# Kernel optimization log

Hardware: AMD Instinct MI355X
Metric: run time of the kernel (lower is better)

## Reference

```python
import math
import jax, jax.numpy as jnp
import numpy as np

D = 1024
NH = 16
DH = D // NH


def setup_inputs() -> dict:
    key = jax.random.key(0)
    k1, k2, k3 = jax.random.split(key, 3)
    x = jax.random.normal(k1, (2, 2048, D), dtype=jnp.float32)
    s = 1.0 / math.sqrt(D)
    W_qkv = jax.random.normal(k2, (D, 3 * D), dtype=jnp.float32) * s
    W_o = jax.random.normal(k3, (D, D), dtype=jnp.float32) * s
    return {"x": x, "W_qkv": W_qkv, "W_o": W_o}


def _rope(q, k, base=10000.0):
    # q, k: [B, H, T, dh]
    half = q.shape[-1] // 2
    freqs = jnp.arange(half, dtype=q.dtype) / half
    theta = 1.0 / base ** freqs                      # [half]
    t = jnp.arange(q.shape[-2], dtype=q.dtype)       # [T]
    ang = t[:, None] * theta[None, :]                # [T, half]
    cos = jnp.cos(ang)[None, None, :, :]
    sin = jnp.sin(ang)[None, None, :, :]

    def rot(x):
        x1, x2 = x[..., :half], x[..., half:]
        return jnp.concatenate([x1 * cos - x2 * sin, x1 * sin + x2 * cos], axis=-1)

    return rot(q), rot(k)


def reference(x, W_qkv, W_o):
    B, T, d = x.shape
    qkv = x @ W_qkv                                   # [B, T, 3D]
    q, k, v = jnp.split(qkv, 3, axis=-1)
    q = q.reshape(B, T, NH, DH).transpose(0, 2, 1, 3)  # [B, H, T, dh]
    k = k.reshape(B, T, NH, DH).transpose(0, 2, 1, 3)
    v = v.reshape(B, T, NH, DH).transpose(0, 2, 1, 3)
    q, k = _rope(q, k)
    att = jnp.einsum('bhtd,bhsd->bhts', q, k) / math.sqrt(DH)  # [B, H, T, T]
    mask = jnp.triu(jnp.full((T, T), -jnp.inf, dtype=att.dtype), 1)
    att = att + mask
    w = jax.nn.softmax(att, axis=-1)
    y = jnp.einsum('bhts,bhsd->bhtd', w, v)           # [B, H, T, dh]
    y = y.transpose(0, 2, 1, 3).reshape(B, T, d)
    return y @ W_o
```

## Files before the change

### kernel.cpp

```cpp
#include <hip/hip_runtime.h>

typedef __bf16 bf16x8 __attribute__((ext_vector_type(8)));
typedef float f32x4 __attribute__((ext_vector_type(4)));
typedef float f32x16 __attribute__((ext_vector_type(16)));

constexpr int SEQ = 2048;
constexpr int DMODEL = 1024;

#define GLL(gp, lp)                                                              \
  __builtin_amdgcn_global_load_lds((const __attribute__((address_space(1))) void*)(gp), \
                                   (__attribute__((address_space(3))) void*)(lp), 16, 0, 0)

__global__ __launch_bounds__(256) void prep_kernel(const float* __restrict__ x,
                                                   const float* __restrict__ Wqkv,
                                                   const float* __restrict__ Wo,
                                                   __bf16* __restrict__ xbf,
                                                   __bf16* __restrict__ WqkvT,
                                                   __bf16* __restrict__ WoT,
                                                   float2* __restrict__ sct) {
  __shared__ __bf16 tile[64][72];
  int blk = blockIdx.x, t = threadIdx.x;

  if (blk < 256) {
    int i = blk * 256 + t;
    int tt = i >> 5, j = i & 31;
    float theta = exp2f(-(float)j * 0.41524101186092953f);
    float s, c;
    __sincosf((float)tt * theta, &s, &c);
    sct[i] = make_float2(c, s);
    return;
  }
  if (blk >= 1280) {
    size_t i = (size_t)(blk - 1280) * 256 + t;
    const float* sp = x + i * 8;
    float4 f0 = *reinterpret_cast<const float4*>(sp);
    float4 f1 = *reinterpret_cast<const float4*>(sp + 4);
    alignas(16) __bf16 tmp[8];
    tmp[0] = (__bf16)f0.x; tmp[1] = (__bf16)f0.y; tmp[2] = (__bf16)f0.z; tmp[3] = (__bf16)f0.w;
    tmp[4] = (__bf16)f1.x; tmp[5] = (__bf16)f1.y; tmp[6] = (__bf16)f1.z; tmp[7] = (__bf16)f1.w;
    *reinterpret_cast<uint4*>(xbf + i * 8) = *reinterpret_cast<const uint4*>(tmp);
    return;
  }
  const float* src;
  __bf16* dst;
  int C, R, c0, r0;
  if (blk < 512) {
    int idx = blk - 256;
    src = Wo; dst = WoT; R = 1024; C = 1024;
    c0 = (idx & 15) * 64; r0 = (idx >> 4) * 64;
  } else {
    int idx = blk - 512;
    src = Wqkv; dst = WqkvT; R = 1024; C = 3072;
    c0 = (idx % 48) * 64; r0 = (idx / 48) * 64;
  }
#pragma unroll
  for (int p = 0; p < 2; ++p) {
    int flat = p * 256 + t;
    int i = flat >> 3;
    int j8 = (flat & 7) * 8;
    const float* sp = &src[(size_t)(r0 + i) * C + c0 + j8];
    float4 f0 = *reinterpret_cast<const float4*>(sp);
    float4 f1 = *reinterpret_cast<const float4*>(sp + 4);
    tile[i][j8 + 0] = (__bf16)f0.x; tile[i][j8 + 1] = (__bf16)f0.y;
    tile[i][j8 + 2] = (__bf16)f0.z; tile[i][j8 + 3] = (__bf16)f0.w;
    tile[i][j8 + 4] = (__bf16)f1.x; tile[i][j8 + 5] = (__bf16)f1.y;
    tile[i][j8 + 6] = (__bf16)f1.z; tile[i][j8 + 7] = (__bf16)f1.w;
  }
  __syncthreads();
#pragma unroll
  for (int p = 0; p < 2; ++p) {
    int flat = p * 256 + t;
    int i = flat >> 3;
    int j8 = (flat & 7) * 8;
    alignas(16) __bf16 tmp[8];
#pragma unroll
    for (int jj = 0; jj < 8; ++jj) tmp[jj] = tile[j8 + jj][i];
    *reinterpret_cast<uint4*>(&dst[(size_t)(c0 + i) * R + r0 + j8]) =
        *reinterpret_cast<const uint4*>(tmp);
  }
}

template <typename CT, int BN, int MODE>
__global__ __launch_bounds__(512, 6) void gemm_bt_lds(const __bf16* __restrict__ A,
                                                      const __bf16* __restrict__ BT,
                                                      CT* __restrict__ C,
                                                      int M, int N, int K, int lda, int ldc,
                                                      const float2* __restrict__ sct,
                                                      __bf16* __restrict__ vt) {
  constexpr int NF = BN / 32;
  __shared__ __align__(16) __bf16 AB_lds[128 + BN][64];
  __bf16 (*A_lds)[64] = &AB_lds[0];
  __bf16 (*B_lds)[64] = &AB_lds[128];

  int tid = threadIdx.x;
  int lane = tid & 63, w = tid >> 6;
  int g = lane >> 4, l15 = lane & 15;
  int wr = w & 3;
  int wc = w >> 2;
  int m0 = blockIdx.x * 128;
  int n0 = blockIdx.y * BN;
  int r8 = lane >> 3;
  int cxe = 8 * ((lane & 7) ^ r8);

  const __bf16* ag = A + (size_t)(m0 + w * 16 + r8) * lda + cxe;
  const __bf16* bg = BT + (size_t)(n0 + w * (BN / 8) + r8) * K + cxe;

  int sxa = 8 * (l15 & 7);

  f32x4 acc[2][NF] = {};

  for (int k0 = 0; k0 < K; k0 += 64) {
    __syncthreads();
    GLL(ag + k0, &A_lds[w * 16][0]);
    GLL(ag + (size_t)8 * lda + k0, &A_lds[w * 16 + 8][0]);
    if constexpr (BN == 128) {
      GLL(bg + k0, &B_lds[w * 16][0]);
      GLL(bg + (size_t)8 * K + k0, &B_lds[w * 16 + 8][0]);
    } else {
      GLL(bg + k0, &B_lds[w * 8][0]);
    }
    __syncthreads();
#pragma unroll
    for (int kk = 0; kk < 2; ++kk) {
      int col = (kk * 32 + g * 8) ^ sxa;
      bf16x8 a[2], bb[NF];
#pragma unroll
      for (int m = 0; m < 2; ++m)
        a[m] = *reinterpret_cast<const bf16x8*>(&A_lds[wr * 32 + m * 16 + l15][col]);
#pragma unroll
      for (int n = 0; n < NF; ++n)
        bb[n] = *reinterpret_cast<const bf16x8*>(&B_lds[wc * (BN / 2) + n * 16 + l15][col]);
#pragma unroll
      for (int m = 0; m < 2; ++m)
#pragma unroll
        for (int n = 0; n < NF; ++n)
          acc[m][n] = __builtin_amdgcn_mfma_f32_16x16x32_bf16(a[m], bb[n], acc[m][n], 0, 0, 0);
    }
  }

  if constexpr (MODE == 3) {
    if (n0 >= 2048) {
      __bf16 (*T_lds)[72] = reinterpret_cast<__bf16(*)[72]>(&AB_lds[0][0]);
      int b = m0 >> 11;
      int s_base = m0 & (SEQ - 1);
#pragma unroll
      for (int half = 0; half < 2; ++half) {
        __syncthreads();
        if (wc == half) {
#pragma unroll
          for (int m = 0; m < 2; ++m)
#pragma unroll
            for (int n = 0; n < NF; ++n)
#pragma unroll
              for (int r = 0; r < 4; ++r)
                T_lds[wr * 32 + m * 16 + 4 * g + r][n * 16 + l15] = (__bf16)acc[m][n][r];
        }
        __syncthreads();
        int head = ((n0 - 2048) >> 6) + half;
        int bh = b * 16 + head;
        int d = tid >> 3;
        int s8 = (tid & 7) * 16;
        __bf16* dst = vt + (size_t)bh * 64 * SEQ + (size_t)d * SEQ + s_base + s8;
#pragma unroll
        for (int j = 0; j < 2; ++j) {
          alignas(16) __bf16 tmp[8];
#pragma unroll
          for (int e = 0; e < 8; ++e) tmp[e] = T_lds[s8 + j * 8 + e][d];
          *reinterpret_cast<uint4*>(dst + j * 8) = *reinterpret_cast<const uint4*>(tmp);
        }
      }
      return;
    }
    bool isq = (n0 < 1024);
    float sc = isq ? 0.18033688011112042f : 1.0f;
#pragma unroll
    for (int m = 0; m < 2; ++m)
#pragma unroll
      for (int r = 0; r < 4; ++r) {
        int row = m0 + wr * 32 + m * 16 + 4 * g + r;
        int t = row & (SEQ - 1);
#pragma unroll
        for (int n = 0; n < 2; ++n) {
          int j = n * 16 + l15;
          float2 cs = sct[(t << 5) + j];
          float x1 = acc[m][n][r], x2 = acc[m][n + 2][r];
          acc[m][n][r]     = (x1 * cs.x - x2 * cs.y) * sc;
          acc[m][n + 2][r] = (x1 * cs.y + x2 * cs.x) * sc;
        }
      }
  }

#pragma unroll
  for (int m = 0; m < 2; ++m)
#pragma unroll
    for (int n = 0; n < NF; ++n)
#pragma unroll
      for (int r = 0; r < 4; ++r) {
        int row = m0 + wr * 32 + m * 16 + 4 * g + r;
        int col = n0 + wc * (BN / 2) + n * 16 + l15;
        C[(size_t)row * ldc + col] = (CT)acc[m][n][r];
      }
}

__device__ inline uint32_t pkbf(float a, float b) {
  union { __bf16 h[2]; uint32_t u; } z;
  z.h[0] = (__bf16)a; z.h[1] = (__bf16)b;
  return z.u;
}

__device__ inline __bf16* slot_base(int gi, __bf16* qkv, __bf16* xbf, int q_local) {
  if (gi < 1024)
    return qkv + (size_t)(gi * 4 + (q_local >> 4)) * 3072 + 2048 + (q_local & 15) * 64;
  return xbf + (size_t)(gi - 1024) * 4096 + (size_t)q_local * 64;
}

__global__ __launch_bounds__(128, 3) void attn_kernel(__bf16* __restrict__ qkv,
                                                      const __bf16* __restrict__ vt,
                                                      __bf16* __restrict__ xbf,
                                                      float* __restrict__ pml) {
  __shared__ __align__(16) __bf16 K_lds[2][64][64];

  int tid = threadIdx.x;
  int w = tid >> 6, lane = tid & 63;
  int l31 = lane & 31, hi = lane >> 5;
  int bid = blockIdx.x;
  int it = bid >> 5, bh = bid & 31;
  int b = bh >> 4, h = bh & 15;

  int qc = 31 - (it >> 1);
  int half = it & 1;
  int NTf = qc + 1;
  int hs = (NTf + 1) >> 1;
  int kv0 = half ? hs : 0;
  int kv1 = half ? NTf : hs;
  int NT = kv1 - kv0;

  __bf16* qbase = qkv + (size_t)b * SEQ * 3072 + h * 64;
  const __bf16* kbase = qbase + 1024;
  const __bf16* vtb = vt + (size_t)bh * 64 * SEQ;

  int q_g = qc * 64 + w * 32 + l31;

  int r8 = lane >> 3;
  int cxe = 8 * ((lane & 7) ^ r8);

  auto STAGE = [&](int bufv, int t) {
#pragma unroll
    for (int i = 0; i < 4; ++i) {
      int R = w * 32 + i * 8;
      GLL(kbase + (size_t)(t * 64 + R + r8) * 3072 + cxe, &K_lds[bufv][R][0]);
    }
  };

  bf16x8 qf[4];
#pragma unroll
  for (int ds = 0; ds < 4; ++ds)
    qf[ds] = *reinterpret_cast<const bf16x8*>(qbase + (size_t)q_g * 3072 + ds * 16 + 8 * hi);

  f32x16 oacc[2] = {};
  float l_run = 0.f;
  const float MFIX = 8.0f;

  if (NT > 0) STAGE(0, kv0);
  __syncthreads();

  int buf = 0;
  for (int jb = 0; jb < NT; ++jb) {
    int kt_g = kv0 + jb;
    bool pre = (jb + 1 < NT);
    if (pre) STAGE(buf ^ 1, kt_g + 1);

    uint4 vr[8];
#pragma unroll
    for (int dt = 0; dt < 2; ++dt)
#pragma unroll
      for (int ks = 0; ks < 4; ++ks)
        vr[dt * 4 + ks] = *reinterpret_cast<const uint4*>(
            vtb + (size_t)(dt * 32 + l31) * SEQ + kt_g * 64 + ks * 16 + 8 * hi);

    f32x16 sacc[2] = {};
    __builtin_amdgcn_s_setprio(1);
#pragma unroll
    for (int kt = 0; kt < 2; ++kt) {
#pragma unroll
      for (int ds = 0; ds < 4; ++ds) {
        bf16x8 kf = *reinterpret_cast<const bf16x8*>(
            &K_lds[buf][kt * 32 + l31][(ds * 16 + 8 * hi) ^ ((l31 & 7) * 8)]);
        sacc[kt] = __builtin_amdgcn_mfma_f32_32x32x16_bf16(kf, qf[ds], sacc[kt], 0, 0, 0);
      }
    }
    __builtin_amdgcn_s_setprio(0);

    if (kt_g == qc) {
#pragma unroll
      for (int kt = 0; kt < 2; ++kt)
#pragma unroll
        for (int r = 0; r < 16; ++r) {
          int k_g = kt_g * 64 + kt * 32 + (r & 3) + 8 * (r >> 2) + 4 * hi;
          if (k_g > q_g) sacc[kt][r] = -1e30f;
        }
    }

    float s0 = 0.f, s1 = 0.f, s2 = 0.f, s3 = 0.f;
#pragma unroll
    for (int kt = 0; kt < 2; ++kt) {
#pragma unroll
      for (int r = 0; r < 16; r += 4) {
        float p0 = exp2f(sacc[kt][r + 0] - MFIX);
        float p1 = exp2f(sacc[kt][r + 1] - MFIX);
        float p2 = exp2f(sacc[kt][r + 2] - MFIX);
        float p3 = exp2f(sacc[kt][r + 3] - MFIX);
        sacc[kt][r + 0] = p0; sacc[kt][r + 1] = p1;
        sacc[kt][r + 2] = p2; sacc[kt][r + 3] = p3;
        s0 += p0; s1 += p1; s2 += p2; s3 += p3;
      }
    }
    float sum = (s0 + s1) + (s2 + s3);
    sum += __shfl_xor(sum, 32);
    l_run += sum;

    uint4 pa[4];
#pragma unroll
    for (int ks = 0; ks < 4; ++ks) {
      int v0 = 2 * ks, v1 = v0 + 1;
      int t0 = v0 >> 2, rb0 = 4 * (v0 & 3);
      int t1 = v1 >> 2, rb1 = 4 * (v1 & 3);
      uint32_t a01, a23, b01, b23;
      if (t0 == 0) { a01 = pkbf(sacc[0][rb0 + 0], sacc[0][rb0 + 1]);
                     a23 = pkbf(sacc[0][rb0 + 2], sacc[0][rb0 + 3]); }
      else         { a01 = pkbf(sacc[1][rb0 + 0], sacc[1][rb0 + 1]);
                     a23 = pkbf(sacc[1][rb0 + 2], sacc[1][rb0 + 3]); }
      if (t1 == 0) { b01 = pkbf(sacc[0][rb1 + 0], sacc[0][rb1 + 1]);
                     b23 = pkbf(sacc[0][rb1 + 2], sacc[0][rb1 + 3]); }
      else         { b01 = pkbf(sacc[1][rb1 + 0], sacc[1][rb1 + 1]);
                     b23 = pkbf(sacc[1][rb1 + 2], sacc[1][rb1 + 3]); }
      uint32_t t01 = hi ? a01 : b01;
      uint32_t t23 = hi ? a23 : b23;
      uint32_t r01 = __shfl_xor(t01, 32);
      uint32_t r23 = __shfl_xor(t23, 32);
      uint32_t k01 = hi ? b01 : a01;
      uint32_t k23 = hi ? b23 : a23;
      pa[ks].x = hi ? r01 : k01;
      pa[ks].y = hi ? r23 : k23;
      pa[ks].z = hi ? k01 : r01;
      pa[ks].w = hi ? k23 : r23;
    }

    __builtin_amdgcn_s_setprio(1);
#pragma unroll
    for (int dt = 0; dt < 2; ++dt) {
#pragma unroll
      for (int ks = 0; ks < 4; ++ks) {
        oacc[dt] = __builtin_amdgcn_mfma_f32_32x32x16_bf16(
            *reinterpret_cast<const bf16x8*>(&vr[dt * 4 + ks]),
            *reinterpret_cast<const bf16x8*>(&pa[ks]), oacc[dt], 0, 0, 0);
      }
    }
    __builtin_amdgcn_s_setprio(0);

    if (pre) {
      asm volatile("s_waitcnt vmcnt(0)" ::: "memory");
      __syncthreads();
    }
    buf ^= 1;
  }

  int gi = ((31 - qc) * 2 + half) * 32 + bh;
  int q_local = w * 32 + l31;
  __bf16* pobase = slot_base(gi, qkv, xbf, q_local);
#pragma unroll
  for (int dt = 0; dt < 2; ++dt)
#pragma unroll
    for (int u = 0; u < 4; ++u) {
      int d0 = dt * 32 + 8 * u + 4 * hi;
      alignas(8) __bf16 tmp[4];
#pragma unroll
      for (int m = 0; m < 4; ++m) tmp[m] = (__bf16)oacc[dt][4 * u + m];
      *reinterpret_cast<uint2*>(pobase + d0) = *reinterpret_cast<const uint2*>(tmp);
    }
  if (hi == 0) pml[gi * 128 + q_local] = l_run;
}

__global__ __launch_bounds__(128) void combine_kernel(__bf16* __restrict__ qkv,
                                                      __bf16* __restrict__ xbf,
                                                      const float* __restrict__ pml) {
  int bid = blockIdx.x;
  int qc = 31 - (bid >> 5), bh = bid & 31;
  int b = bh >> 4, h = bh & 15;
  int t = threadIdx.x;
  int q = t >> 1, dh = (t & 1) * 32;

  int g0 = ((31 - qc) * 2 + 0) * 32 + bh;
  int g1 = g0 + 32;
  float l0 = pml[g0 * 128 + q];
  float l1 = pml[g1 * 128 + q];
  float inv = 1.0f / (l0 + l1);

  const __bf16* p0 = slot_base(g0, qkv, xbf, q) + dh;
  const __bf16* p1 = slot_base(g1, qkv, xbf, q) + dh;
  __bf16* yq = qkv + (size_t)(b * SEQ + qc * 64 + q) * 3072 + h * 64 + dh;

#pragma unroll
  for (int c = 0; c < 4; ++c) {
    uint4 ua = *reinterpret_cast<const uint4*>(p0 + c * 8);
    uint4 ub = *reinterpret_cast<const uint4*>(p1 + c * 8);
    const __bf16* va = reinterpret_cast<const __bf16*>(&ua);
    const __bf16* vb = reinterpret_cast<const __bf16*>(&ub);
    alignas(16) __bf16 outv[8];
#pragma unroll
    for (int j = 0; j < 8; ++j)
      outv[j] = (__bf16)((((float)va[j]) + ((float)vb[j])) * inv);
    *reinterpret_cast<uint4*>(yq + c * 8) = *reinterpret_cast<const uint4*>(outv);
  }
}

extern "C" void kernel_launch(void* const* d_in, const int* in_sizes, int n_in,
                              void* d_out, int out_size, void* d_ws, size_t ws_size,
                              hipStream_t stream) {
  const float* x = (const float*)d_in[0];
  const float* Wqkv = (const float*)d_in[1];
  const float* Wo = (const float*)d_in[2];
  float* out = (float*)d_out;

  __bf16* ws = (__bf16*)d_ws;
  __bf16* WqkvT = ws;
  __bf16* WoT = WqkvT + (size_t)3072 * 1024;
  __bf16* qkv = WoT + (size_t)1024 * 1024;
  __bf16* xbf = qkv + (size_t)4096 * 3072;
  __bf16* vtb = xbf + (size_t)4096 * 1024;
  float* pml = (float*)(vtb + (size_t)32 * 64 * SEQ);
  float2* sct = (float2*)(pml + 2048 * 128);

  prep_kernel<<<3328, 256, 0, stream>>>(x, Wqkv, Wo, xbf, WqkvT, WoT, sct);

  gemm_bt_lds<__bf16, 128, 3><<<dim3(32, 24), 512, 0, stream>>>(
      xbf, WqkvT, qkv, 4096, 3072, 1024, 1024, 3072, sct, vtb);

  attn_kernel<<<2048, 128, 0, stream>>>(qkv, vtb, xbf, pml);

  combine_kernel<<<1024, 128, 0, stream>>>(qkv, xbf, pml);

  gemm_bt_lds<float, 64, 0><<<dim3(32, 16), 512, 0, stream>>>(
      qkv, WoT, out, 4096, 1024, 1024, 3072, 1024, sct, nullptr);
}
```

Before: 118.8 us.

## Load K tiles directly from global into registers, drop LDS double buffer

```diff
diff --git a/kernel.cpp b/kernel.cpp
--- a/kernel.cpp
+++ b/kernel.cpp
@@ -214,12 +214,10 @@
   return xbf + (size_t)(gi - 1024) * 4096 + (size_t)q_local * 64;
 }
 
-__global__ __launch_bounds__(128, 3) void attn_kernel(__bf16* __restrict__ qkv,
+__global__ __launch_bounds__(128, 4) void attn_kernel(__bf16* __restrict__ qkv,
                                                       const __bf16* __restrict__ vt,
                                                       __bf16* __restrict__ xbf,
                                                       float* __restrict__ pml) {
-  __shared__ __align__(16) __bf16 K_lds[2][64][64];
-
   int tid = threadIdx.x;
   int w = tid >> 6, lane = tid & 63;
   int l31 = lane & 31, hi = lane >> 5;
@@ -241,17 +239,6 @@
 
   int q_g = qc * 64 + w * 32 + l31;
 
-  int r8 = lane >> 3;
-  int cxe = 8 * ((lane & 7) ^ r8);
-
-  auto STAGE = [&](int bufv, int t) {
-#pragma unroll
-    for (int i = 0; i < 4; ++i) {
-      int R = w * 32 + i * 8;
-      GLL(kbase + (size_t)(t * 64 + R + r8) * 3072 + cxe, &K_lds[bufv][R][0]);
-    }
-  };
-
   bf16x8 qf[4];
 #pragma unroll
   for (int ds = 0; ds < 4; ++ds)
@@ -261,14 +248,27 @@
   float l_run = 0.f;
   const float MFIX = 8.0f;
 
-  if (NT > 0) STAGE(0, kv0);
-  __syncthreads();
-
-  int buf = 0;
+  const __bf16* krow = kbase + (size_t)l31 * 3072 + 8 * hi;
+
   for (int jb = 0; jb < NT; ++jb) {
     int kt_g = kv0 + jb;
-    bool pre = (jb + 1 < NT);
-    if (pre) STAGE(buf ^ 1, kt_g + 1);
+
+    bf16x8 kf[2][4];
+#pragma unroll
+    for (int kt = 0; kt < 2; ++kt)
+#pragma unroll
+      for (int ds = 0; ds < 4; ++ds)
+        kf[kt][ds] = *reinterpret_cast<const bf16x8*>(
+            krow + (size_t)(kt_g * 64 + kt * 32) * 3072 + ds * 16);
+
+    f32x16 sacc[2] = {};
+    __builtin_amdgcn_s_setprio(1);
+#pragma unroll
+    for (int kt = 0; kt < 2; ++kt)
+#pragma unroll
+      for (int ds = 0; ds < 4; ++ds)
+        sacc[kt] = __builtin_amdgcn_mfma_f32_32x32x16_bf16(kf[kt][ds], qf[ds], sacc[kt], 0, 0, 0);
+    __builtin_amdgcn_s_setprio(0);
 
     uint4 vr[8];
 #pragma unroll
@@ -277,19 +277,6 @@
       for (int ks = 0; ks < 4; ++ks)
         vr[dt * 4 + ks] = *reinterpret_cast<const uint4*>(
             vtb + (size_t)(dt * 32 + l31) * SEQ + kt_g * 64 + ks * 16 + 8 * hi);
-
-    f32x16 sacc[2] = {};
-    __builtin_amdgcn_s_setprio(1);
-#pragma unroll
-    for (int kt = 0; kt < 2; ++kt) {
-#pragma unroll
-      for (int ds = 0; ds < 4; ++ds) {
-        bf16x8 kf = *reinterpret_cast<const bf16x8*>(
-            &K_lds[buf][kt * 32 + l31][(ds * 16 + 8 * hi) ^ ((l31 & 7) * 8)]);
-        sacc[kt] = __builtin_amdgcn_mfma_f32_32x32x16_bf16(kf, qf[ds], sacc[kt], 0, 0, 0);
-      }
-    }
-    __builtin_amdgcn_s_setprio(0);
 
     if (kt_g == qc) {
 #pragma unroll
@@ -357,12 +344,6 @@
       }
     }
     __builtin_amdgcn_s_setprio(0);
-
-    if (pre) {
-      asm volatile("s_waitcnt vmcnt(0)" ::: "memory");
-      __syncthreads();
-    }
-    buf ^= 1;
   }
 
   int gi = ((31 - qc) * 2 + half) * 32 + bh;
```

Measured after the change: 147.8 us. 24.4% more time.
